# Optimization experiments

Hardware: AMD Instinct MI355X
Metric: run time of the kernel (lower is better)

The kernel has to match this reference:

```python
import jax, jax.numpy as jnp
import numpy as np

B, T, C = 2, 2048, 2048
N_HEAD, N_GROUPS, HEAD_SIZE = 16, 4, 128
Q_PER_KV = N_HEAD // N_GROUPS


def setup_inputs() -> dict:
    key = jax.random.key(0)
    k1, k2, k3 = jax.random.split(key, 3)
    x = jax.random.normal(k1, (B, T, C), dtype=jnp.float32)
    # real RoPE cache: theta_i = 10000^{-2i/d}, cos/sin of shape [T, head_size//2]
    half = HEAD_SIZE // 2
    inv_freq = 1.0 / (10000.0 ** (jnp.arange(0, half, dtype=jnp.float32) / half))
    t = jnp.arange(T, dtype=jnp.float32)
    freqs = t[:, None] * inv_freq[None, :]  # [T, half]
    cos, sin = jnp.cos(freqs), jnp.sin(freqs)
    w_attn = jax.random.normal(k2, (C, (N_HEAD + 2 * N_GROUPS) * HEAD_SIZE), dtype=jnp.float32) * (C ** -0.5)
    w_proj = jax.random.normal(k3, (C, C), dtype=jnp.float32) * (C ** -0.5)
    return {"x": x, "cos": cos, "sin": sin, "w_attn": w_attn, "w_proj": w_proj}


def _apply_rope(x, cos, sin):
    # flash-attn style, interleaved=False: rotate first/second half of rotary dims
    # x: [B, T, H, D], cos/sin: [T, D//2]
    d2 = cos.shape[-1]
    x1, x2 = x[..., :d2], x[..., d2:2 * d2]
    c = cos[None, :, None, :]
    s = sin[None, :, None, :]
    return jnp.concatenate([x1 * c - x2 * s, x1 * s + x2 * c], axis=-1)


def reference(x, cos, sin, w_attn, w_proj):
    Bx, Tx, Cx = x.shape
    qkv = x @ w_attn  # [B, T, (n_head + 2*G)*hs]
    qkv = qkv.reshape(Bx, Tx, N_GROUPS, Q_PER_KV + 2, HEAD_SIZE)
    q = qkv[:, :, :, :Q_PER_KV, :].reshape(Bx, Tx, N_HEAD, HEAD_SIZE)
    k = qkv[:, :, :, Q_PER_KV, :]        # [B, T, G, hs]
    v = qkv[:, :, :, Q_PER_KV + 1, :]    # [B, T, G, hs]
    q = _apply_rope(q, cos, sin)
    k = _apply_rope(k, cos, sin)
    # GQA attention without materializing repeated K/V
    qg = q.reshape(Bx, Tx, N_GROUPS, Q_PER_KV, HEAD_SIZE)
    scale = 1.0 / jnp.sqrt(jnp.float32(HEAD_SIZE))
    scores = jnp.einsum('bqgpd,bkgd->bgpqk', qg, k) * scale  # [B,G,p,T,T]
    attn = jax.nn.softmax(scores, axis=-1)
    y = jnp.einsum('bgpqk,bkgd->bqgpd', attn, v)  # [B,T,G,p,hs]
    y = y.reshape(Bx, Tx, Cx)
    return y @ w_proj
```

## Files before the change

kernel.cpp:

```cpp
#include <hip/hip_runtime.h>
#include <stdint.h>

#define B_ 2
#define T_ 2048
#define C_ 2048
#define NH 16
#define NG 4
#define HS 128

typedef unsigned short u16;
typedef __bf16 bf16_t;
typedef bf16_t bf16x8 __attribute__((ext_vector_type(8)));
typedef float f32x4 __attribute__((ext_vector_type(4)));

__device__ __forceinline__ u16 f2bf(float f) {
    union { float f; uint32_t u; } v; v.f = f;
    uint32_t r = (v.u + 0x7fffu + ((v.u >> 16) & 1u)) >> 16;
    return (u16)r;
}
__device__ __forceinline__ float bf2f(u16 h) {
    union { uint32_t u; float f; } v; v.u = ((uint32_t)h) << 16;
    return v.f;
}

__device__ __forceinline__ void transpose_body(const float* __restrict__ W, u16* __restrict__ Wt,
                                               int K, int N, int bx, int by, float (*tile)[33]) {
    int n0 = bx * 32, k0 = by * 32;
    int tx = threadIdx.x & 31, ty = threadIdx.x >> 5;
#pragma unroll
    for (int i = 0; i < 4; i++) {
        int r = ty + i * 8;
        tile[r][tx] = W[(size_t)(k0 + r) * N + (n0 + tx)];
    }
    __syncthreads();
#pragma unroll
    for (int i = 0; i < 4; i++) {
        int r = ty + i * 8;
        Wt[(size_t)(n0 + r) * K + (k0 + tx)] = f2bf(tile[tx][r]);
    }
}

__global__ void k_prep(const float* __restrict__ x, u16* __restrict__ xb,
                       const float* __restrict__ wa, u16* __restrict__ wat,
                       const float* __restrict__ wp, u16* __restrict__ wpt) {
    __shared__ float tile[32][33];
    int bid = blockIdx.x;
    if (bid < 8192) {
        int i = bid * 256 + threadIdx.x;
        float4 f = ((const float4*)x)[i];
        ushort4 o;
        o.x = f2bf(f.x); o.y = f2bf(f.y); o.z = f2bf(f.z); o.w = f2bf(f.w);
        ((ushort4*)xb)[i] = o;
    } else if (bid < 8192 + 6144) {
        int id = bid - 8192;
        transpose_body(wa, wat, 2048, 3072, id % 96, id / 96, tile);
    } else {
        int id = bid - 14336;
        transpose_body(wp, wpt, 2048, 2048, id % 64, id / 64, tile);
    }
}

#define MIDB { __builtin_amdgcn_s_barrier();                              \
               asm volatile("s_waitcnt lgkmcnt(0)" ::: "memory");         \
               __builtin_amdgcn_sched_barrier(0); }
#define ENDB { __builtin_amdgcn_s_barrier(); }
#define VMW4 { asm volatile("s_waitcnt vmcnt(4)" ::: "memory"); }
#define VMW0 { asm volatile("s_waitcnt vmcnt(0)" ::: "memory"); }

__device__ __forceinline__ void stage_half(const u16* __restrict__ g, int r0, int k0,
                                           u16* l, int tid) {
#pragma unroll
    for (int i = 0; i < 2; i++) {
        int c = tid + i * 512;
        int row = c >> 3, sl = c & 7;
        const u16* ga = g + (size_t)(r0 + row) * 2048 + k0 + (sl ^ (row & 7)) * 8;
        __builtin_amdgcn_global_load_lds((const __attribute__((address_space(1))) void*)ga,
                                         (__attribute__((address_space(3))) void*)(l + c * 8),
                                         16, 0, 0);
    }
}

__device__ __forceinline__ void rd_a(const u16* slot, int mq, int l16, int quad,
                                     bf16x8 (&af)[4][2]) {
#pragma unroll
    for (int mf = 0; mf < 4; mf++) {
        int row = mq * 64 + mf * 16 + l16;
#pragma unroll
        for (int kk = 0; kk < 2; kk++)
            af[mf][kk] = *(const bf16x8*)(slot + row * 64 + ((kk * 4 + quad) ^ (l16 & 7)) * 8);
    }
}

__device__ __forceinline__ void rd_b(const u16* slot, int nq, int wc1, int l16, int quad,
                                     bf16x8 (&bs)[2][2]) {
#pragma unroll
    for (int g = 0; g < 2; g++) {
        int row = wc1 * 64 + (nq * 2 + g) * 16 + l16;
#pragma unroll
        for (int kk = 0; kk < 2; kk++)
            bs[g][kk] = *(const bf16x8*)(slot + row * 64 + ((kk * 4 + quad) ^ (l16 & 7)) * 8);
    }
}

template <int MQ, int NQ>
__device__ __forceinline__ void mm8(f32x4 (&acc)[8][4], const bf16x8 (&af)[4][2],
                                    const bf16x8 (&bs)[2][2]) {
    __builtin_amdgcn_s_setprio(1);
#pragma unroll
    for (int mf = 0; mf < 4; mf++)
#pragma unroll
        for (int g = 0; g < 2; g++)
#pragma unroll
            for (int kk = 0; kk < 2; kk++)
                acc[MQ * 4 + mf][NQ * 2 + g] = __builtin_amdgcn_mfma_f32_16x16x32_bf16(
                    af[mf][kk], bs[g][kk], acc[MQ * 4 + mf][NQ * 2 + g], 0, 0, 0);
    __builtin_amdgcn_s_setprio(0);
}

__global__ __launch_bounds__(512, 2) void k_gemm_qkv(const u16* __restrict__ A,
                                                     const u16* __restrict__ Bt,
                                                     const float* __restrict__ cosb,
                                                     const float* __restrict__ sinb,
                                                     u16* __restrict__ qa,
                                                     u16* __restrict__ ka,
                                                     u16* __restrict__ vt) {
    extern __shared__ __align__(16) u16 sm[];
    const int tid = threadIdx.x;
    const int wave = tid >> 6, lane = tid & 63;
    const int quad = lane >> 4, l16 = lane & 15;
    const int wr = wave >> 2, wc = wave & 3;
    const int m0 = blockIdx.y * 256;
    const int brow = blockIdx.x * 256;

    const u16* As0 = sm + (0 * 2 + wr) * 8192;
    const u16* As1 = sm + (1 * 2 + wr) * 8192;
    const u16* Bs0 = sm + 32768 + (0 * 2 + (wc >> 1)) * 8192;
    const u16* Bs1 = sm + 32768 + (1 * 2 + (wc >> 1)) * 8192;

    f32x4 acc[8][4] = {};
    bf16x8 af[4][2], b0[2][2], b1[2][2];

    stage_half(A,  m0,        0,  sm + 0 * 8192, tid);
    stage_half(A,  m0 + 128,  0,  sm + 1 * 8192, tid);
    stage_half(Bt, brow,       0,  sm + 32768 + 0 * 8192, tid);
    stage_half(Bt, brow + 128, 0,  sm + 32768 + 1 * 8192, tid);
    stage_half(Bt, brow,       64, sm + 32768 + 2 * 8192, tid);
    stage_half(Bt, brow + 128, 64, sm + 32768 + 3 * 8192, tid);
    VMW4;
    __builtin_amdgcn_s_barrier();

    for (int i = 0; i < 15; i++) {
        const int k0 = i * 128;
        rd_a(As0, 0, l16, quad, af); rd_b(Bs0, 0, wc & 1, l16, quad, b0);
        stage_half(A, m0, k0 + 64, sm + 2 * 8192, tid);
        MIDB; mm8<0, 0>(acc, af, b0); ENDB;
        rd_b(Bs0, 1, wc & 1, l16, quad, b1);
        stage_half(A, m0 + 128, k0 + 64, sm + 3 * 8192, tid);
        MIDB; mm8<0, 1>(acc, af, b1); ENDB;
        rd_a(As0, 1, l16, quad, af);
        stage_half(Bt, brow, k0 + 128, sm + 32768 + 0 * 8192, tid);
        MIDB; mm8<1, 1>(acc, af, b1); ENDB;
        stage_half(Bt, brow + 128, k0 + 128, sm + 32768 + 1 * 8192, tid);
        MIDB; mm8<1, 0>(acc, af, b0); VMW4; ENDB;
        rd_a(As1, 0, l16, quad, af); rd_b(Bs1, 0, wc & 1, l16, quad, b0);
        stage_half(A, m0, k0 + 128, sm + 0 * 8192, tid);
        MIDB; mm8<0, 0>(acc, af, b0); ENDB;
        rd_b(Bs1, 1, wc & 1, l16, quad, b1);
        stage_half(A, m0 + 128, k0 + 128, sm + 1 * 8192, tid);
        MIDB; mm8<0, 1>(acc, af, b1); ENDB;
        rd_a(As1, 1, l16, quad, af);
        stage_half(Bt, brow, k0 + 192, sm + 32768 + 2 * 8192, tid);
        MIDB; mm8<1, 1>(acc, af, b1); ENDB;
        stage_half(Bt, brow + 128, k0 + 192, sm + 32768 + 3 * 8192, tid);
        MIDB; mm8<1, 0>(acc, af, b0); VMW4; ENDB;
    }
    {
        rd_a(As0, 0, l16, quad, af); rd_b(Bs0, 0, wc & 1, l16, quad, b0);
        stage_half(A, m0, 1984, sm + 2 * 8192, tid);
        MIDB; mm8<0, 0>(acc, af, b0); ENDB;
        rd_b(Bs0, 1, wc & 1, l16, quad, b1);
        stage_half(A, m0 + 128, 1984, sm + 3 * 8192, tid);
        MIDB; mm8<0, 1>(acc, af, b1); ENDB;
        rd_a(As0, 1, l16, quad, af);
        MIDB; mm8<1, 1>(acc, af, b1); ENDB;
        MIDB; mm8<1, 0>(acc, af, b0); VMW0; ENDB;
        rd_a(As1, 0, l16, quad, af); rd_b(Bs1, 0, wc & 1, l16, quad, b0);
        MIDB; mm8<0, 0>(acc, af, b0); ENDB;
        rd_b(Bs1, 1, wc & 1, l16, quad, b1);
        MIDB; mm8<0, 1>(acc, af, b1); ENDB;
        rd_a(As1, 1, l16, quad, af);
        MIDB; mm8<1, 1>(acc, af, b1); ENDB;
        MIDB; mm8<1, 0>(acc, af, b0); ENDB;
    }

    __syncthreads();
    const int s = blockIdx.x * 2 + (wc >> 1);
    const int stype = s % 6, grp = s / 6;
    const int dhalf = wc & 1;
    const int b = blockIdx.y >> 3;
    const int tb = (blockIdx.y & 7) * 256 + wr * 128;
    const int rid = wr * 2 + (wc >> 1);
    float4* xch = (float4*)sm;

    if (stype < 5 && dhalf == 1) {
#pragma unroll
        for (int mf = 0; mf < 8; mf++)
#pragma unroll
            for (int g = 0; g < 4; g++)
                xch[((rid * 8 + mf) * 4 + g) * 64 + quad * 16 + l16] = *(float4*)&acc[mf][g];
    }
    __syncthreads();
    if (stype < 5) {
        if (dhalf == 0) {
            const float QS = 0.08838834764831845f * 1.44269504088896341f;
            const float sc = (stype < 4) ? QS : 1.0f;
            u16* dst = (stype < 4) ? qa + ((size_t)(b * NH + grp * 4 + stype)) * T_ * 128
                                   : ka + ((size_t)(b * NG + grp)) * T_ * 128;
#pragma unroll
            for (int mf = 0; mf < 8; mf++)
#pragma unroll
                for (int g = 0; g < 4; g++) {
                    float4 x2 = xch[((rid * 8 + mf) * 4 + g) * 64 + quad * 16 + l16];
                    const float* x2p = (const float*)&x2;
                    int d = g * 16 + l16;
#pragma unroll
                    for (int r = 0; r < 4; r++) {
                        int t = tb + mf * 16 + quad * 4 + r;
                        float cc = cosb[t * 64 + d], ss = sinb[t * 64 + d];
                        float x1 = acc[mf][g][r];
                        u16* drow = dst + (size_t)t * 128;
                        drow[d] = f2bf((x1 * cc - x2p[r] * ss) * sc);
                        drow[d + 64] = f2bf((x1 * ss + x2p[r] * cc) * sc);
                    }
                }
        }
    } else {
        size_t vb = ((size_t)(b * NG + grp)) * 128;
#pragma unroll
        for (int mf = 0; mf < 8; mf++)
#pragma unroll
            for (int g = 0; g < 4; g++) {
                int d = dhalf * 64 + g * 16 + l16;
                int t0 = tb + mf * 16 + quad * 4;
                ushort4 o = make_ushort4(f2bf(acc[mf][g][0]), f2bf(acc[mf][g][1]),
                                         f2bf(acc[mf][g][2]), f2bf(acc[mf][g][3]));
                *(ushort4*)(vt + (vb + d) * T_ + t0) = o;
            }
    }
}

__global__ __launch_bounds__(256) void k_gemm_bt(const u16* __restrict__ A,
                                                 const u16* __restrict__ Bt,
                                                 float* __restrict__ C,
                                                 int M, int N, int K) {
    __shared__ __align__(16) u16 As[128 * 32];
    __shared__ __align__(16) u16 Bs[128 * 32];
    const int tid = threadIdx.x;
    const int wave = tid >> 6, lane = tid & 63;
    const int quad = lane >> 4, l16 = lane & 15;
    const int wr = wave >> 1, wc = wave & 1;
    const int m0 = blockIdx.y * 128, n0 = blockIdx.x * 128;

    f32x4 acc[4][4] = {};

    for (int k0 = 0; k0 < K; k0 += 32) {
        __syncthreads();
#pragma unroll
        for (int i = 0; i < 2; i++) {
            int c = tid + i * 256;
            int row = c >> 2, seg = c & 3;
            const u16* ga = A + (size_t)(m0 + row) * K + k0 + seg * 8;
            const u16* gb = Bt + (size_t)(n0 + row) * K + k0 + seg * 8;
            __builtin_amdgcn_global_load_lds((const __attribute__((address_space(1))) void*)ga,
                                             (__attribute__((address_space(3))) void*)&As[c * 8],
                                             16, 0, 0);
            __builtin_amdgcn_global_load_lds((const __attribute__((address_space(1))) void*)gb,
                                             (__attribute__((address_space(3))) void*)&Bs[c * 8],
                                             16, 0, 0);
        }
        __syncthreads();
        bf16x8 a[4], b[4];
#pragma unroll
        for (int mi = 0; mi < 4; mi++)
            a[mi] = *(const bf16x8*)&As[(wr * 64 + mi * 16 + l16) * 32 + quad * 8];
#pragma unroll
        for (int ni = 0; ni < 4; ni++)
            b[ni] = *(const bf16x8*)&Bs[(wc * 64 + ni * 16 + l16) * 32 + quad * 8];
#pragma unroll
        for (int mi = 0; mi < 4; mi++)
#pragma unroll
            for (int ni = 0; ni < 4; ni++)
                acc[mi][ni] = __builtin_amdgcn_mfma_f32_16x16x32_bf16(a[mi], b[ni], acc[mi][ni], 0, 0, 0);
    }
#pragma unroll
    for (int mi = 0; mi < 4; mi++)
#pragma unroll
        for (int ni = 0; ni < 4; ni++)
#pragma unroll
            for (int r = 0; r < 4; r++) {
                int row = m0 + wr * 64 + mi * 16 + quad * 4 + r;
                int col = n0 + wc * 64 + ni * 16 + l16;
                C[(size_t)row * N + col] = acc[mi][ni][r];
            }
}

__global__ __launch_bounds__(256, 2) void k_attn(const u16* __restrict__ qa,
                                                 const u16* __restrict__ ka,
                                                 const u16* __restrict__ vt,
                                                 u16* __restrict__ ya) {
    __shared__ __align__(16) u16 smem[32768];
    const int tid = threadIdx.x;
    const int wave = tid >> 6, lane = tid & 63;
    const int quad = lane >> 4, l16 = lane & 15;
    const int qt = blockIdx.x, h = blockIdx.y, b = blockIdx.z;
    const int g = h >> 2;

    bf16x8 qf[2][4];
    {
        const u16* qbase = qa + (((size_t)(b * NH + h)) * T_ + qt * 128 + wave * 32 + l16) * 128;
#pragma unroll
        for (int t16 = 0; t16 < 2; t16++)
#pragma unroll
            for (int ks = 0; ks < 4; ks++)
                qf[t16][ks] = *(const bf16x8*)(qbase + t16 * 16 * 128 + ks * 32 + quad * 8);
    }
    const u16* kbase = ka + ((size_t)(b * NG + g)) * T_ * 128;
    const u16* vbase = vt + ((size_t)(b * NG + g)) * 128 * T_;

    f32x4 yacc[2][8] = {};
    float lsum[2] = {0.f, 0.f};
    uint4 vr[4];

#pragma unroll
    for (int i = 0; i < 4; i++) {
        int c = tid + i * 256;
        int row = c >> 4, seg = c & 15;
        const u16* gk = kbase + (size_t)row * 128 + (seg ^ (row & 15)) * 8;
        __builtin_amdgcn_global_load_lds((const __attribute__((address_space(1))) void*)gk,
                                         (__attribute__((address_space(3))) void*)(smem + c * 8),
                                         16, 0, 0);
    }
#pragma unroll
    for (int i = 0; i < 4; i++) {
        int p = tid + i * 256;
        int d = p >> 3, m = p & 7;
        vr[i] = *(const uint4*)(vbase + (size_t)d * T_ + m * 8);
    }

    for (int kt = 0; kt < T_ / 64; kt++) {
        const int cur = kt & 1;
        u16* Kc = smem + cur * 8192;
        u16* Vc = smem + 16384 + cur * 8192;

        asm volatile("s_waitcnt vmcnt(0)" ::: "memory");
#pragma unroll
        for (int i = 0; i < 4; i++) {
            int p = tid + i * 256;
            int d = p >> 3, m = p & 7;
            int segA = (m >> 2) * 4 + (m & 1) * 2;
            int a4 = ((m >> 1) & 1) * 4;
            *(uint2*)&Vc[d * 64 + (segA ^ (d & 7)) * 8 + a4] = make_uint2(vr[i].x, vr[i].y);
            *(uint2*)&Vc[d * 64 + ((segA + 1) ^ (d & 7)) * 8 + a4] = make_uint2(vr[i].z, vr[i].w);
        }
        __syncthreads();

        if (kt + 1 < T_ / 64) {
            u16* Kn = smem + (cur ^ 1) * 8192;
#pragma unroll
            for (int i = 0; i < 4; i++) {
                int c = tid + i * 256;
                int row = c >> 4, seg = c & 15;
                const u16* gk = kbase + (size_t)((kt + 1) * 64 + row) * 128 + (seg ^ (row & 15)) * 8;
                __builtin_amdgcn_global_load_lds((const __attribute__((address_space(1))) void*)gk,
                                                 (__attribute__((address_space(3))) void*)(Kn + c * 8),
                                                 16, 0, 0);
            }
#pragma unroll
            for (int i = 0; i < 4; i++) {
                int p = tid + i * 256;
                int d = p >> 3, m = p & 7;
                vr[i] = *(const uint4*)(vbase + (size_t)d * T_ + (kt + 1) * 64 + m * 8);
            }
        }

        f32x4 sacc[2][4] = {};
        __builtin_amdgcn_s_setprio(1);
#pragma unroll
        for (int ks = 0; ks < 4; ks++) {
#pragma unroll
            for (int ni = 0; ni < 4; ni++) {
                bf16x8 kf = *(const bf16x8*)&Kc[(ni * 16 + l16) * 128 + ((ks * 4 + quad) ^ l16) * 8];
                sacc[0][ni] = __builtin_amdgcn_mfma_f32_16x16x32_bf16(kf, qf[0][ks], sacc[0][ni], 0, 0, 0);
                sacc[1][ni] = __builtin_amdgcn_mfma_f32_16x16x32_bf16(kf, qf[1][ks], sacc[1][ni], 0, 0, 0);
            }
        }
        __builtin_amdgcn_s_setprio(0);

        uint32_t pk[2][4][2];
#pragma unroll
        for (int t16 = 0; t16 < 2; t16++) {
#pragma unroll
            for (int ni = 0; ni < 4; ni++) {
                float p0 = exp2f(sacc[t16][ni][0]);
                float p1 = exp2f(sacc[t16][ni][1]);
                float p2 = exp2f(sacc[t16][ni][2]);
                float p3 = exp2f(sacc[t16][ni][3]);
                lsum[t16] += (p0 + p1) + (p2 + p3);
                asm("v_cvt_pk_bf16_f32 %0, %1, %2" : "=v"(pk[t16][ni][0]) : "v"(p0), "v"(p1));
                asm("v_cvt_pk_bf16_f32 %0, %1, %2" : "=v"(pk[t16][ni][1]) : "v"(p2), "v"(p3));
            }
        }

        __builtin_amdgcn_s_setprio(1);
#pragma unroll
        for (int ks2 = 0; ks2 < 2; ks2++) {
            union { uint32_t u[4]; bf16x8 v; } pf0, pf1;
            pf0.u[0] = pk[0][2 * ks2][0];     pf0.u[1] = pk[0][2 * ks2][1];
            pf0.u[2] = pk[0][2 * ks2 + 1][0]; pf0.u[3] = pk[0][2 * ks2 + 1][1];
            pf1.u[0] = pk[1][2 * ks2][0];     pf1.u[1] = pk[1][2 * ks2][1];
            pf1.u[2] = pk[1][2 * ks2 + 1][0]; pf1.u[3] = pk[1][2 * ks2 + 1][1];
#pragma unroll
            for (int tile = 0; tile < 8; tile++) {
                bf16x8 vf = *(const bf16x8*)&Vc[(tile * 16 + l16) * 64 +
                                                ((ks2 * 4 + quad) ^ (l16 & 7)) * 8];
                yacc[0][tile] = __builtin_amdgcn_mfma_f32_16x16x32_bf16(vf, pf0.v, yacc[0][tile], 0, 0, 0);
                yacc[1][tile] = __builtin_amdgcn_mfma_f32_16x16x32_bf16(vf, pf1.v, yacc[1][tile], 0, 0, 0);
            }
        }
        __builtin_amdgcn_s_setprio(0);
    }

#pragma unroll
    for (int t16 = 0; t16 < 2; t16++) {
        lsum[t16] += __shfl_xor(lsum[t16], 16);
        lsum[t16] += __shfl_xor(lsum[t16], 32);
    }

    __syncthreads();
#pragma unroll
    for (int t16 = 0; t16 < 2; t16++) {
        float inv = 1.f / lsum[t16];
        int qrow = wave * 32 + t16 * 16 + l16;
#pragma unroll
        for (int tile = 0; tile < 8; tile++) {
#pragma unroll
            for (int cp = 0; cp < 2; cp++) {
                int d = tile * 16 + quad * 4 + cp * 2;
                uint32_t pv = (uint32_t)f2bf(yacc[t16][tile][cp * 2] * inv) |
                              ((uint32_t)f2bf(yacc[t16][tile][cp * 2 + 1] * inv) << 16);
                *(uint32_t*)&smem[qrow * 128 + ((d >> 3) ^ l16) * 8 + (d & 7)] = pv;
            }
        }
    }
    __syncthreads();
#pragma unroll
    for (int i = 0; i < 8; i++) {
        int cc = tid + i * 256;
        int row = cc >> 4, seg = cc & 15;
        uint4 dv = *(const uint4*)&smem[row * 128 + (seg ^ (row & 15)) * 8];
        size_t q = (size_t)(b * T_ + qt * 128 + row);
        *(uint4*)(ya + q * C_ + h * 128 + seg * 8) = dv;
    }
}

extern "C" void kernel_launch(void* const* d_in, const int* in_sizes, int n_in,
                              void* d_out, int out_size, void* d_ws, size_t ws_size,
                              hipStream_t stream) {
    (void)in_sizes; (void)n_in; (void)out_size; (void)ws_size;
    const float* x = (const float*)d_in[0];
    const float* cosb = (const float*)d_in[1];
    const float* sinb = (const float*)d_in[2];
    const float* w_attn = (const float*)d_in[3];
    const float* w_proj = (const float*)d_in[4];
    float* out = (float*)d_out;

    char* ws = (char*)d_ws;
    size_t off = 0;
    auto alloc = [&](size_t bytes) -> char* {
        char* p = ws + off;
        off += (bytes + 255) & ~(size_t)255;
        return p;
    };
    u16* xb  = (u16*)alloc((size_t)4096 * 2048 * 2);
    u16* wat = (u16*)alloc((size_t)3072 * 2048 * 2);
    u16* wpt = (u16*)alloc((size_t)2048 * 2048 * 2);
    u16* qa  = (u16*)alloc((size_t)B_ * NH * T_ * HS * 2);
    u16* ka  = (u16*)alloc((size_t)B_ * NG * T_ * HS * 2);
    u16* vt  = (u16*)alloc((size_t)B_ * NG * T_ * HS * 2);
    u16* ya  = xb;

    static bool smset = false;
    if (!smset) {
        (void)hipFuncSetAttribute((const void*)k_gemm_qkv,
                                  hipFuncAttributeMaxDynamicSharedMemorySize, 131072);
        smset = true;
    }

    k_prep<<<dim3(18432), dim3(256), 0, stream>>>(x, xb, w_attn, wat, w_proj, wpt);
    k_gemm_qkv<<<dim3(12, 16), dim3(512), 131072, stream>>>(xb, wat, cosb, sinb, qa, ka, vt);
    k_attn<<<dim3(16, 16, 2), dim3(256), 0, stream>>>(qa, ka, vt, ya);
    k_gemm_bt<<<dim3(16, 32), dim3(256), 0, stream>>>(ya, wpt, out, 4096, 2048, 2048);
}
```

Baseline: 315.8 us.

## Pipeline output projection GEMM with swizzled double-buffered LDS and raw exp2

Replaces the simple output-projection GEMM with a 512-thread, 128x256-tile kernel. It uses double-buffered swizzled LDS staging that overlaps global loads with MFMA work, in the same style as the QKV GEMM. The attention kernel now precomputes its K/V load and store offsets once instead of every iteration, and uses the raw v_exp_f32 instruction in place of exp2f. The GEMM change is meant to hide load latency and cut per-iteration barriers. It costs more LDS and hardcodes the problem dimensions, and the raw exp drops denormal handling.

```diff
diff --git a/kernel.cpp b/kernel.cpp
--- a/kernel.cpp
+++ b/kernel.cpp
@@ -18,9 +18,8 @@
     uint32_t r = (v.u + 0x7fffu + ((v.u >> 16) & 1u)) >> 16;
     return (u16)r;
 }
-__device__ __forceinline__ float bf2f(u16 h) {
-    union { uint32_t u; float f; } v; v.u = ((uint32_t)h) << 16;
-    return v.f;
+__device__ __forceinline__ float fast_ex2(float x) {
+    float r; asm("v_exp_f32 %0, %1" : "=v"(r) : "v"(x)); return r;
 }
 
 __device__ __forceinline__ void transpose_body(const float* __restrict__ W, u16* __restrict__ Wt,
@@ -80,6 +79,15 @@
     }
 }
 
+__device__ __forceinline__ void stage_half64(const u16* __restrict__ g, int r0, int k0,
+                                             u16* l, int tid) {
+    int row = tid >> 3, sl = tid & 7;
+    const u16* ga = g + (size_t)(r0 + row) * 2048 + k0 + (sl ^ (row & 7)) * 8;
+    __builtin_amdgcn_global_load_lds((const __attribute__((address_space(1))) void*)ga,
+                                     (__attribute__((address_space(3))) void*)(l + tid * 8),
+                                     16, 0, 0);
+}
+
 __device__ __forceinline__ void rd_a(const u16* slot, int mq, int l16, int quad,
                                      bf16x8 (&af)[4][2]) {
 #pragma unroll
@@ -91,11 +99,11 @@
     }
 }
 
-__device__ __forceinline__ void rd_b(const u16* slot, int nq, int wc1, int l16, int quad,
+__device__ __forceinline__ void rd_b(const u16* slot, int nq, int sub, int l16, int quad,
                                      bf16x8 (&bs)[2][2]) {
 #pragma unroll
     for (int g = 0; g < 2; g++) {
-        int row = wc1 * 64 + (nq * 2 + g) * 16 + l16;
+        int row = sub * 64 + (nq * 2 + g) * 16 + l16;
 #pragma unroll
         for (int kk = 0; kk < 2; kk++)
             bs[g][kk] = *(const bf16x8*)(slot + row * 64 + ((kk * 4 + quad) ^ (l16 & 7)) * 8);
@@ -114,6 +122,21 @@
             for (int kk = 0; kk < 2; kk++)
                 acc[MQ * 4 + mf][NQ * 2 + g] = __builtin_amdgcn_mfma_f32_16x16x32_bf16(
                     af[mf][kk], bs[g][kk], acc[MQ * 4 + mf][NQ * 2 + g], 0, 0, 0);
+    __builtin_amdgcn_s_setprio(0);
+}
+
+template <int MQ, int NQ>
+__device__ __forceinline__ void mm4(f32x4 (&acc)[4][4], const bf16x8 (&af)[2][2],
+                                    const bf16x8 (&bs)[2][2]) {
+    __builtin_amdgcn_s_setprio(1);
+#pragma unroll
+    for (int mf = 0; mf < 2; mf++)
+#pragma unroll
+        for (int g = 0; g < 2; g++)
+#pragma unroll
+            for (int kk = 0; kk < 2; kk++)
+                acc[MQ * 2 + mf][NQ * 2 + g] = __builtin_amdgcn_mfma_f32_16x16x32_bf16(
+                    af[mf][kk], bs[g][kk], acc[MQ * 2 + mf][NQ * 2 + g], 0, 0, 0);
     __builtin_amdgcn_s_setprio(0);
 }
 
@@ -249,58 +272,87 @@
     }
 }
 
-__global__ __launch_bounds__(256) void k_gemm_bt(const u16* __restrict__ A,
-                                                 const u16* __restrict__ Bt,
-                                                 float* __restrict__ C,
-                                                 int M, int N, int K) {
-    __shared__ __align__(16) u16 As[128 * 32];
-    __shared__ __align__(16) u16 Bs[128 * 32];
+__global__ __launch_bounds__(512, 2) void k_gemm_bt(const u16* __restrict__ A,
+                                                    const u16* __restrict__ Bt,
+                                                    float* __restrict__ C) {
+    extern __shared__ __align__(16) u16 sm[];
     const int tid = threadIdx.x;
     const int wave = tid >> 6, lane = tid & 63;
     const int quad = lane >> 4, l16 = lane & 15;
-    const int wr = wave >> 1, wc = wave & 1;
-    const int m0 = blockIdx.y * 128, n0 = blockIdx.x * 128;
+    const int wr = wave >> 2, wc = wave & 3;
+    const int bh = wc >> 1, sub = wc & 1;
+    const int m0 = blockIdx.y * 128, n0 = blockIdx.x * 256;
+
+    const u16* As0 = sm + (0 * 2 + wr) * 4096;
+    const u16* As1 = sm + (1 * 2 + wr) * 4096;
+    const u16* Bs0 = sm + 16384 + (0 * 2 + bh) * 8192;
+    const u16* Bs1 = sm + 16384 + (1 * 2 + bh) * 8192;
 
     f32x4 acc[4][4] = {};
-
-    for (int k0 = 0; k0 < K; k0 += 32) {
-        __syncthreads();
-#pragma unroll
-        for (int i = 0; i < 2; i++) {
-            int c = tid + i * 256;
-            int row = c >> 2, seg = c & 3;
-            const u16* ga = A + (size_t)(m0 + row) * K + k0 + seg * 8;
-            const u16* gb = Bt + (size_t)(n0 + row) * K + k0 + seg * 8;
-            __builtin_amdgcn_global_load_lds((const __attribute__((address_space(1))) void*)ga,
-                                             (__attribute__((address_space(3))) void*)&As[c * 8],
-                                             16, 0, 0);
-            __builtin_amdgcn_global_load_lds((const __attribute__((address_space(1))) void*)gb,
-                                             (__attribute__((address_space(3))) void*)&Bs[c * 8],
-                                             16, 0, 0);
-        }
-        __syncthreads();
-        bf16x8 a[4], b[4];
-#pragma unroll
-        for (int mi = 0; mi < 4; mi++)
-            a[mi] = *(const bf16x8*)&As[(wr * 64 + mi * 16 + l16) * 32 + quad * 8];
-#pragma unroll
-        for (int ni = 0; ni < 4; ni++)
-            b[ni] = *(const bf16x8*)&Bs[(wc * 64 + ni * 16 + l16) * 32 + quad * 8];
-#pragma unroll
-        for (int mi = 0; mi < 4; mi++)
-#pragma unroll
-            for (int ni = 0; ni < 4; ni++)
-                acc[mi][ni] = __builtin_amdgcn_mfma_f32_16x16x32_bf16(a[mi], b[ni], acc[mi][ni], 0, 0, 0);
-    }
-#pragma unroll
-    for (int mi = 0; mi < 4; mi++)
-#pragma unroll
-        for (int ni = 0; ni < 4; ni++)
+    bf16x8 af[2][2], b0[2][2], b1[2][2];
+
+    stage_half64(A, m0,       0, sm + 0 * 4096, tid);
+    stage_half64(A, m0 + 64,  0, sm + 1 * 4096, tid);
+    stage_half(Bt, n0,        0, sm + 16384 + 0 * 8192, tid);
+    stage_half(Bt, n0 + 128,  0, sm + 16384 + 1 * 8192, tid);
+    stage_half(Bt, n0,       64, sm + 16384 + 2 * 8192, tid);
+    stage_half(Bt, n0 + 128, 64, sm + 16384 + 3 * 8192, tid);
+    VMW4;
+    __builtin_amdgcn_s_barrier();
+
+    for (int i = 0; i < 15; i++) {
+        const int k0 = i * 128;
+        rd_b(As0, 0, 0, l16, quad, af); rd_b(Bs0, 0, sub, l16, quad, b0);
+        stage_half64(A, m0, k0 + 64, sm + 2 * 4096, tid);
+        MIDB; mm4<0, 0>(acc, af, b0); ENDB;
+        rd_b(Bs0, 1, sub, l16, quad, b1);
+        stage_half64(A, m0 + 64, k0 + 64, sm + 3 * 4096, tid);
+        MIDB; mm4<0, 1>(acc, af, b1); ENDB;
+        rd_b(As0, 1, 0, l16, quad, af);
+        stage_half(Bt, n0, k0 + 128, sm + 16384 + 0 * 8192, tid);
+        MIDB; mm4<1, 1>(acc, af, b1); ENDB;
+        stage_half(Bt, n0 + 128, k0 + 128, sm + 16384 + 1 * 8192, tid);
+        MIDB; mm4<1, 0>(acc, af, b0); VMW4; ENDB;
+        rd_b(As1, 0, 0, l16, quad, af); rd_b(Bs1, 0, sub, l16, quad, b0);
+        stage_half64(A, m0, k0 + 128, sm + 0 * 4096, tid);
+        MIDB; mm4<0, 0>(acc, af, b0); ENDB;
+        rd_b(Bs1, 1, sub, l16, quad, b1);
+        stage_half64(A, m0 + 64, k0 + 128, sm + 1 * 4096, tid);
+        MIDB; mm4<0, 1>(acc, af, b1); ENDB;
+        rd_b(As1, 1, 0, l16, quad, af);
+        stage_half(Bt, n0, k0 + 192, sm + 16384 + 2 * 8192, tid);
+        MIDB; mm4<1, 1>(acc, af, b1); ENDB;
+        stage_half(Bt, n0 + 128, k0 + 192, sm + 16384 + 3 * 8192, tid);
+        MIDB; mm4<1, 0>(acc, af, b0); VMW4; ENDB;
+    }
+    {
+        rd_b(As0, 0, 0, l16, quad, af); rd_b(Bs0, 0, sub, l16, quad, b0);
+        stage_half64(A, m0, 1984, sm + 2 * 4096, tid);
+        MIDB; mm4<0, 0>(acc, af, b0); ENDB;
+        rd_b(Bs0, 1, sub, l16, quad, b1);
+        stage_half64(A, m0 + 64, 1984, sm + 3 * 4096, tid);
+        MIDB; mm4<0, 1>(acc, af, b1); ENDB;
+        rd_b(As0, 1, 0, l16, quad, af);
+        MIDB; mm4<1, 1>(acc, af, b1); ENDB;
+        MIDB; mm4<1, 0>(acc, af, b0); VMW0; ENDB;
+        rd_b(As1, 0, 0, l16, quad, af); rd_b(Bs1, 0, sub, l16, quad, b0);
+        MIDB; mm4<0, 0>(acc, af, b0); ENDB;
+        rd_b(Bs1, 1, sub, l16, quad, b1);
+        MIDB; mm4<0, 1>(acc, af, b1); ENDB;
+        rd_b(As1, 1, 0, l16, quad, af);
+        MIDB; mm4<1, 1>(acc, af, b1); ENDB;
+        MIDB; mm4<1, 0>(acc, af, b0); ENDB;
+    }
+
+#pragma unroll
+    for (int am = 0; am < 4; am++)
+#pragma unroll
+        for (int an = 0; an < 4; an++)
 #pragma unroll
             for (int r = 0; r < 4; r++) {
-                int row = m0 + wr * 64 + mi * 16 + quad * 4 + r;
-                int col = n0 + wc * 64 + ni * 16 + l16;
-                C[(size_t)row * N + col] = acc[mi][ni][r];
+                int row = m0 + wr * 64 + am * 16 + quad * 4 + r;
+                int col = n0 + wc * 64 + an * 16 + l16;
+                C[(size_t)row * C_ + col] = acc[am][an][r];
             }
 }
 
@@ -327,25 +379,33 @@
     const u16* kbase = ka + ((size_t)(b * NG + g)) * T_ * 128;
     const u16* vbase = vt + ((size_t)(b * NG + g)) * 128 * T_;
 
+    int kdst[4], ksrc[4], vsrc[4], vdA[4], vdB[4];
+#pragma unroll
+    for (int i = 0; i < 4; i++) {
+        int c = tid + i * 256;
+        int row = c >> 4, seg = c & 15;
+        kdst[i] = c * 8;
+        ksrc[i] = row * 128 + (seg ^ (row & 15)) * 8;
+        int d = c >> 3, m = c & 7;
+        vsrc[i] = d * T_ + m * 8;
+        int segA = (m >> 2) * 4 + (m & 1) * 2;
+        int a4 = ((m >> 1) & 1) * 4;
+        vdA[i] = d * 64 + (segA ^ (d & 7)) * 8 + a4;
+        vdB[i] = d * 64 + ((segA + 1) ^ (d & 7)) * 8 + a4;
+    }
+
     f32x4 yacc[2][8] = {};
     float lsum[2] = {0.f, 0.f};
     uint4 vr[4];
 
 #pragma unroll
-    for (int i = 0; i < 4; i++) {
-        int c = tid + i * 256;
-        int row = c >> 4, seg = c & 15;
-        const u16* gk = kbase + (size_t)row * 128 + (seg ^ (row & 15)) * 8;
-        __builtin_amdgcn_global_load_lds((const __attribute__((address_space(1))) void*)gk,
-                                         (__attribute__((address_space(3))) void*)(smem + c * 8),
+    for (int i = 0; i < 4; i++)
+        __builtin_amdgcn_global_load_lds((const __attribute__((address_space(1))) void*)(kbase + ksrc[i]),
+                                         (__attribute__((address_space(3))) void*)(smem + kdst[i]),
                                          16, 0, 0);
-    }
-#pragma unroll
-    for (int i = 0; i < 4; i++) {
-        int p = tid + i * 256;
-        int d = p >> 3, m = p & 7;
-        vr[i] = *(const uint4*)(vbase + (size_t)d * T_ + m * 8);
-    }
+#pragma unroll
+    for (int i = 0; i < 4; i++)
+        vr[i] = *(const uint4*)(vbase + vsrc[i]);
 
     for (int kt = 0; kt < T_ / 64; kt++) {
         const int cur = kt & 1;
@@ -355,32 +415,23 @@
         asm volatile("s_waitcnt vmcnt(0)" ::: "memory");
 #pragma unroll
         for (int i = 0; i < 4; i++) {
-            int p = tid + i * 256;
-            int d = p >> 3, m = p & 7;
-            int segA = (m >> 2) * 4 + (m & 1) * 2;
-            int a4 = ((m >> 1) & 1) * 4;
-            *(uint2*)&Vc[d * 64 + (segA ^ (d & 7)) * 8 + a4] = make_uint2(vr[i].x, vr[i].y);
-            *(uint2*)&Vc[d * 64 + ((segA + 1) ^ (d & 7)) * 8 + a4] = make_uint2(vr[i].z, vr[i].w);
+            *(uint2*)&Vc[vdA[i]] = make_uint2(vr[i].x, vr[i].y);
+            *(uint2*)&Vc[vdB[i]] = make_uint2(vr[i].z, vr[i].w);
         }
         __syncthreads();
 
         if (kt + 1 < T_ / 64) {
             u16* Kn = smem + (cur ^ 1) * 8192;
-#pragma unroll
-            for (int i = 0; i < 4; i++) {
-                int c = tid + i * 256;
-                int row = c >> 4, seg = c & 15;
-                const u16* gk = kbase + (size_t)((kt + 1) * 64 + row) * 128 + (seg ^ (row & 15)) * 8;
-                __builtin_amdgcn_global_load_lds((const __attribute__((address_space(1))) void*)gk,
-                                                 (__attribute__((address_space(3))) void*)(Kn + c * 8),
+            const u16* kb = kbase + (size_t)(kt + 1) * 64 * 128;
+#pragma unroll
+            for (int i = 0; i < 4; i++)
+                __builtin_amdgcn_global_load_lds((const __attribute__((address_space(1))) void*)(kb + ksrc[i]),
+                                                 (__attribute__((address_space(3))) void*)(Kn + kdst[i]),
                                                  16, 0, 0);
-            }
-#pragma unroll
-            for (int i = 0; i < 4; i++) {
-                int p = tid + i * 256;
-                int d = p >> 3, m = p & 7;
-                vr[i] = *(const uint4*)(vbase + (size_t)d * T_ + (kt + 1) * 64 + m * 8);
-            }
+            const u16* vb = vbase + (kt + 1) * 64;
+#pragma unroll
+            for (int i = 0; i < 4; i++)
+                vr[i] = *(const uint4*)(vb + vsrc[i]);
         }
 
         f32x4 sacc[2][4] = {};
@@ -401,10 +452,10 @@
         for (int t16 = 0; t16 < 2; t16++) {
 #pragma unroll
             for (int ni = 0; ni < 4; ni++) {
-                float p0 = exp2f(sacc[t16][ni][0]);
-                float p1 = exp2f(sacc[t16][ni][1]);
-                float p2 = exp2f(sacc[t16][ni][2]);
-                float p3 = exp2f(sacc[t16][ni][3]);
+                float p0 = fast_ex2(sacc[t16][ni][0]);
+                float p1 = fast_ex2(sacc[t16][ni][1]);
+                float p2 = fast_ex2(sacc[t16][ni][2]);
+                float p3 = fast_ex2(sacc[t16][ni][3]);
                 lsum[t16] += (p0 + p1) + (p2 + p3);
                 asm("v_cvt_pk_bf16_f32 %0, %1, %2" : "=v"(pk[t16][ni][0]) : "v"(p0), "v"(p1));
                 asm("v_cvt_pk_bf16_f32 %0, %1, %2" : "=v"(pk[t16][ni][1]) : "v"(p2), "v"(p3));
@@ -493,11 +544,13 @@
     if (!smset) {
         (void)hipFuncSetAttribute((const void*)k_gemm_qkv,
                                   hipFuncAttributeMaxDynamicSharedMemorySize, 131072);
+        (void)hipFuncSetAttribute((const void*)k_gemm_bt,
+                                  hipFuncAttributeMaxDynamicSharedMemorySize, 98304);
         smset = true;
     }
 
     k_prep<<<dim3(18432), dim3(256), 0, stream>>>(x, xb, w_attn, wat, w_proj, wpt);
     k_gemm_qkv<<<dim3(12, 16), dim3(512), 131072, stream>>>(xb, wat, cosb, sinb, qa, ka, vt);
     k_attn<<<dim3(16, 16, 2), dim3(256), 0, stream>>>(qa, ka, vt, ya);
-    k_gemm_bt<<<dim3(16, 32), dim3(256), 0, stream>>>(ya, wpt, out, 4096, 2048, 2048);
-}
+    k_gemm_bt<<<dim3(8, 32), dim3(512), 98304, stream>>>(ya, wpt, out);
+}
```

New measurement: 280.9 us. -11.1%, faster.
